# Optimization experiments

Hardware: AMD Instinct MI355X
Metric: run time of the kernel (lower is better)

## Reference

```python
import math
import jax, jax.numpy as jnp
import numpy as np

B, N, D, H = 8, 128, 256, 8
DK = D // H
SCALE = 0.02


def setup_inputs() -> dict:
    key = jax.random.key(0)
    ks = jax.random.split(key, 10)
    return {
        "query_node": jax.random.normal(ks[0], (B, N, D), jnp.float32),
        "value_node": jax.random.normal(ks[1], (B, N, D), jnp.float32),
        "key_edge": jax.random.normal(ks[2], (B, N, N, D), jnp.float32),
        "adj_matrix": jax.random.uniform(ks[3], (B, N, N), jnp.float32),  # pairwise distances >= 0
        "mask": jnp.ones((B, N), jnp.int32),
        "Wq": jax.random.normal(ks[4], (D, D), jnp.float32) * SCALE,
        "bq": jnp.zeros((D,), jnp.float32),
        "Wk": jax.random.normal(ks[5], (D, D), jnp.float32) * SCALE,
        "bk": jnp.zeros((D,), jnp.float32),
        "Wv": jax.random.normal(ks[6], (D, D), jnp.float32) * SCALE,
        "bv": jnp.zeros((D,), jnp.float32),
        "Wno": jax.random.normal(ks[7], (D, D), jnp.float32) * SCALE,
        "bno": jnp.zeros((D,), jnp.float32),
        "Weo": jax.random.normal(ks[8], (D, D), jnp.float32) * SCALE,
        "beo": jnp.zeros((D,), jnp.float32),
        "att_lambda": jnp.float32(0.1),
    }


def reference(query_node, value_node, key_edge, adj_matrix, mask,
              Wq, bq, Wk, bk, Wv, bv, Wno, bno, Weo, beo, att_lambda):
    # distance-kernelized adjacency: softmax(-lambda * dist) over neighbors
    adj = att_lambda * adj_matrix                                  # [B,N,N]
    adj = jnp.where(mask[:, None, :] == 0, jnp.inf, adj)
    adj = jax.nn.softmax(-adj, axis=-1)                            # [B,N,N]

    q = (query_node @ Wq.T + bq).reshape(B, N, H, DK).transpose(0, 2, 1, 3)      # [B,H,N,DK] bhmd
    k = (key_edge @ Wk.T + bk).reshape(B, N, N, H, DK).transpose(0, 3, 1, 2, 4)  # [B,H,N,N,DK] bhmnd
    v = (value_node @ Wv.T + bv).reshape(B, N, H, DK).transpose(0, 2, 1, 3)      # [B,H,N,DK] bhnd

    inv_sqrt = 1.0 / math.sqrt(DK)
    out_scores = jnp.einsum('bhmd,bhmnd->bhmn', q, k) * inv_sqrt
    in_scores = jnp.einsum('bhnd,bhmnd->bhnm', q, k) * inv_sqrt

    m4 = mask[:, None, None, :] == 0                               # [B,1,1,N]
    neg_inf = jnp.asarray(-jnp.inf, out_scores.dtype)
    out_scores = jnp.where(m4, neg_inf, out_scores)
    in_scores = jnp.where(m4, neg_inf, in_scores)

    out_attn = jax.nn.softmax(out_scores, axis=-1)
    in_attn = jax.nn.softmax(in_scores, axis=-1)

    # message = out_attn + in_attn - diag_embed(diag(out_attn))
    eye = jnp.eye(N, dtype=out_attn.dtype)
    message = out_attn + in_attn - out_attn * eye
    message = message * adj[:, None]                               # adjacency gating (dropout = identity at eval)

    node_hidden = jnp.einsum('bhmn,bhnd->bhmd', message, v)        # [B,H,N,DK]
    edge_hidden = message[..., None] * k                           # [B,H,N,N,DK] outer-product edge update

    node_hidden = node_hidden.transpose(0, 2, 1, 3).reshape(B, N, D)
    edge_hidden = edge_hidden.transpose(0, 2, 3, 1, 4).reshape(B, N, N, D)

    return (node_hidden @ Wno.T + bno, edge_hidden @ Weo.T + beo)
```

## Files before the change

kernel.cpp:

```cpp
#include <hip/hip_runtime.h>
#include <math.h>

#define Bc 8
#define Nc 128
#define Dc 256
#define Hc 8
#define DKc 32

typedef __attribute__((ext_vector_type(8))) short short8;
typedef __attribute__((ext_vector_type(4))) float floatx4;

__device__ __forceinline__ unsigned short f2bf(float f) {
  unsigned int u = __float_as_uint(f);
  u += 0x7FFFu + ((u >> 16) & 1u);
  return (unsigned short)(u >> 16);
}

__global__ __launch_bounds__(256) void cast_bf16_kernel(
    const float* __restrict__ src, unsigned short* __restrict__ dst, int n) {
  const int i = (blockIdx.x * 256 + threadIdx.x) * 4;
  if (i < n) {
    const float4 v = *(const float4*)&src[i];
    *(ushort4*)&dst[i] = make_ushort4(f2bf(v.x), f2bf(v.y), f2bf(v.z), f2bf(v.w));
  }
}

__global__ __launch_bounds__(256) void gemm_xwT_kernel(
    const float* __restrict__ X, const float* __restrict__ W,
    const float* __restrict__ bias, float* __restrict__ C, int M) {
  __shared__ float As[64][17];
  __shared__ float Ws[64][17];
  const int t = threadIdx.x;
  const int tx = t & 15;
  const int ty = t >> 4;
  const size_t row0 = (size_t)blockIdx.y * 64;
  const int col0 = blockIdx.x * 64;
  const int lr = t >> 2;
  const int lc = (t & 3) * 4;

  float acc[4][4] = {};

  for (int kk = 0; kk < 256; kk += 16) {
    float4 av = *(const float4*)&X[(row0 + lr) * 256 + kk + lc];
    float4 wv = *(const float4*)&W[(size_t)(col0 + lr) * 256 + kk + lc];
    As[lr][lc] = av.x; As[lr][lc + 1] = av.y; As[lr][lc + 2] = av.z; As[lr][lc + 3] = av.w;
    Ws[lr][lc] = wv.x; Ws[lr][lc + 1] = wv.y; Ws[lr][lc + 2] = wv.z; Ws[lr][lc + 3] = wv.w;
    __syncthreads();
#pragma unroll
    for (int e = 0; e < 16; ++e) {
      float a[4], w[4];
#pragma unroll
      for (int r = 0; r < 4; ++r) a[r] = As[ty * 4 + r][e];
#pragma unroll
      for (int c = 0; c < 4; ++c) w[c] = Ws[tx * 4 + c][e];
#pragma unroll
      for (int r = 0; r < 4; ++r)
#pragma unroll
        for (int c = 0; c < 4; ++c) acc[r][c] = fmaf(a[r], w[c], acc[r][c]);
    }
    __syncthreads();
  }

  const float4 bv = *(const float4*)&bias[col0 + tx * 4];
#pragma unroll
  for (int r = 0; r < 4; ++r) {
    float4 o;
    o.x = acc[r][0] + bv.x;
    o.y = acc[r][1] + bv.y;
    o.z = acc[r][2] + bv.z;
    o.w = acc[r][3] + bv.w;
    *(float4*)&C[(row0 + ty * 4 + r) * 256 + col0 + tx * 4] = o;
  }
}

__global__ __launch_bounds__(256) void kproj_mfma_kernel(
    const float* __restrict__ X, const unsigned short* __restrict__ Wbf,
    const float* __restrict__ bias, float* __restrict__ C) {
  __shared__ __align__(16) unsigned short As[128 * 40];
  __shared__ __align__(16) unsigned short Ws[128 * 40];
  const int t = threadIdx.x;
  const int l = t & 63;
  const int w = t >> 6;
  const int wm = w >> 1, wn = w & 1;
  const size_t row0 = (size_t)blockIdx.y * 128;
  const int col0 = blockIdx.x * 128;
  const int lr = l & 15;
  const int lk = l >> 4;

  floatx4 acc[4][4] = {};

  for (int kk = 0; kk < 256; kk += 32) {
    float4 av[4];
#pragma unroll
    for (int p = 0; p < 4; ++p) {
      const int f = p * 256 + t;
      const int row = f >> 3, kc = (f & 7) * 4;
      av[p] = *(const float4*)&X[(row0 + row) * 256 + kk + kc];
    }
    uint4 wv[2];
#pragma unroll
    for (int p = 0; p < 2; ++p) {
      const int f = p * 256 + t;
      const int row = f >> 2, kc = (f & 3) * 8;
      wv[p] = *(const uint4*)&Wbf[(size_t)(col0 + row) * 256 + kk + kc];
    }
    __syncthreads();
#pragma unroll
    for (int p = 0; p < 4; ++p) {
      const int f = p * 256 + t;
      const int row = f >> 3, kc = (f & 7) * 4;
      *(ushort4*)&As[row * 40 + kc] =
          make_ushort4(f2bf(av[p].x), f2bf(av[p].y), f2bf(av[p].z), f2bf(av[p].w));
    }
#pragma unroll
    for (int p = 0; p < 2; ++p) {
      const int f = p * 256 + t;
      const int row = f >> 2, kc = (f & 3) * 8;
      *(uint4*)&Ws[row * 40 + kc] = wv[p];
    }
    __syncthreads();
    short8 a[4], b[4];
#pragma unroll
    for (int i = 0; i < 4; ++i)
      a[i] = *(const short8*)&As[(wm * 64 + i * 16 + lr) * 40 + lk * 8];
#pragma unroll
    for (int j = 0; j < 4; ++j)
      b[j] = *(const short8*)&Ws[(wn * 64 + j * 16 + lr) * 40 + lk * 8];
#pragma unroll
    for (int i = 0; i < 4; ++i)
#pragma unroll
      for (int j = 0; j < 4; ++j)
        acc[i][j] = __builtin_amdgcn_mfma_f32_16x16x32_bf16(a[i], b[j], acc[i][j], 0, 0, 0);
  }

  float bj[4];
#pragma unroll
  for (int j = 0; j < 4; ++j) bj[j] = bias[col0 + wn * 64 + j * 16 + lr];
#pragma unroll
  for (int i = 0; i < 4; ++i)
#pragma unroll
    for (int r = 0; r < 4; ++r) {
      const size_t row = row0 + wm * 64 + i * 16 + lk * 4 + r;
#pragma unroll
      for (int j = 0; j < 4; ++j)
        C[row * 256 + col0 + wn * 64 + j * 16 + lr] = acc[i][j][r] + bj[j];
    }
}

__global__ __launch_bounds__(128) void adj_softmax_kernel(
    const float* __restrict__ adj, const int* __restrict__ mask,
    const float* __restrict__ lam_p, float* __restrict__ adjs) {
  __shared__ float red[128];
  const int bi = blockIdx.x;
  const int b = bi >> 7;
  const int j = threadIdx.x;
  const float lam = lam_p[0];
  float x = (mask[b * 128 + j] != 0) ? (-lam * adj[(size_t)bi * 128 + j]) : -INFINITY;
  red[j] = x; __syncthreads();
  for (int s = 64; s > 0; s >>= 1) { if (j < s) red[j] = fmaxf(red[j], red[j + s]); __syncthreads(); }
  const float mx = red[0]; __syncthreads();
  const float e = expf(x - mx);
  red[j] = e; __syncthreads();
  for (int s = 64; s > 0; s >>= 1) { if (j < s) red[j] += red[j + s]; __syncthreads(); }
  const float z = red[0];
  adjs[(size_t)bi * 128 + j] = e / z;
}

__global__ __launch_bounds__(256) void scores_kernel(
    const float* __restrict__ kbuf, const float* __restrict__ q,
    float* __restrict__ osc, float* __restrict__ isc) {
  const int bm = blockIdx.x;
  const int b = bm >> 7;
  const int m = bm & 127;
  const int lane = threadIdx.x & 63;
  const int wave = threadIdx.x >> 6;
  const float inv_sqrt = 0.17677669529663687f;

  const float4 qm = *(const float4*)&q[((size_t)b * 128 + m) * 256 + lane * 4];

  for (int n = wave; n < 128; n += 4) {
    const float4 kr = *(const float4*)&kbuf[((size_t)bm * 128 + n) * 256 + lane * 4];
    const float4 qn = *(const float4*)&q[((size_t)b * 128 + n) * 256 + lane * 4];
    float po = kr.x * qm.x + kr.y * qm.y + kr.z * qm.z + kr.w * qm.w;
    float pi = kr.x * qn.x + kr.y * qn.y + kr.z * qn.z + kr.w * qn.w;
#pragma unroll
    for (int off = 1; off < 8; off <<= 1) {
      po += __shfl_xor(po, off, 64);
      pi += __shfl_xor(pi, off, 64);
    }
    if ((lane & 7) == 0) {
      const int h = lane >> 3;
      osc[(((size_t)(b * 8 + h) * 128 + m) * 128) + n] = po * inv_sqrt;
      isc[(((size_t)(b * 8 + h) * 128 + n) * 128) + m] = pi * inv_sqrt;
    }
  }
}

__global__ __launch_bounds__(128) void message_kernel(
    const float* __restrict__ osc, const float* __restrict__ isc,
    const float* __restrict__ adjs, const int* __restrict__ mask,
    float* __restrict__ msg) {
  __shared__ float red[128];
  const int bhi = blockIdx.x;
  const int i = bhi & 127;
  const int b = bhi >> 10;
  const int j = threadIdx.x;
  const bool mj = mask[b * 128 + j] != 0;

  const float so = mj ? osc[(size_t)bhi * 128 + j] : -INFINITY;
  const float si = mj ? isc[(size_t)bhi * 128 + j] : -INFINITY;

  red[j] = so; __syncthreads();
  for (int s = 64; s > 0; s >>= 1) { if (j < s) red[j] = fmaxf(red[j], red[j + s]); __syncthreads(); }
  const float mo = red[0]; __syncthreads();
  const float eo = expf(so - mo);
  red[j] = eo; __syncthreads();
  for (int s = 64; s > 0; s >>= 1) { if (j < s) red[j] += red[j + s]; __syncthreads(); }
  const float zo = red[0]; __syncthreads();
  const float oa = eo / zo;

  red[j] = si; __syncthreads();
  for (int s = 64; s > 0; s >>= 1) { if (j < s) red[j] = fmaxf(red[j], red[j + s]); __syncthreads(); }
  const float mi = red[0]; __syncthreads();
  const float ei = expf(si - mi);
  red[j] = ei; __syncthreads();
  for (int s = 64; s > 0; s >>= 1) { if (j < s) red[j] += red[j + s]; __syncthreads(); }
  const float zi = red[0];
  const float ia = ei / zi;

  float val = oa + ia - ((i == j) ? oa : 0.0f);
  val *= adjs[((size_t)(b * 128 + i)) * 128 + j];
  msg[(size_t)bhi * 128 + j] = val;
}

__global__ __launch_bounds__(256) void node_hidden_kernel(
    const float* __restrict__ msg, const float* __restrict__ v,
    float* __restrict__ nh) {
  __shared__ float Ms[32][129];
  __shared__ float Vs[128][33];
  const int blk = blockIdx.x;
  const int mblk = blk & 3;
  const int bh = blk >> 2;
  const int h = bh & 7;
  const int b = bh >> 3;
  const int t = threadIdx.x;

  {
    const int n = t & 127, r0 = t >> 7;
#pragma unroll
    for (int p = 0; p < 16; ++p) {
      const int r = r0 + p * 2;
      Ms[r][n] = msg[((size_t)bh * 128 + mblk * 32 + r) * 128 + n];
    }
  }
  {
    const int dk = t & 31, n0 = t >> 5;
#pragma unroll
    for (int p = 0; p < 16; ++p) {
      const int n = n0 + p * 8;
      Vs[n][dk] = v[((size_t)b * 128 + n) * 256 + h * 32 + dk];
    }
  }
  __syncthreads();

  const int dk = t & 31;
  const int mg = t >> 5;
  float acc[4] = {0.f, 0.f, 0.f, 0.f};
  for (int n = 0; n < 128; ++n) {
    const float vv = Vs[n][dk];
#pragma unroll
    for (int r = 0; r < 4; ++r) acc[r] = fmaf(Ms[mg + 8 * r][n], vv, acc[r]);
  }
#pragma unroll
  for (int r = 0; r < 4; ++r) {
    const int m = mblk * 32 + mg + 8 * r;
    nh[((size_t)b * 128 + m) * 256 + h * 32 + dk] = acc[r];
  }
}

__global__ __launch_bounds__(256) void edge_mfma_kernel(
    float* __restrict__ kio, const float* __restrict__ msg,
    const unsigned short* __restrict__ Wbf, const float* __restrict__ beo) {
  __shared__ __align__(16) unsigned short As[64 * 40];
  __shared__ __align__(16) unsigned short Ws[256 * 40];
  __shared__ float Msgs[64][8];
  const int nblk = blockIdx.x;
  const int bm = blockIdx.y;
  const int b = bm >> 7;
  const int m = bm & 127;
  const int n0 = nblk * 64;
  const int t = threadIdx.x;
  const int l = t & 63;
  const int w = t >> 6;
  const int lr = l & 15;
  const int lk = l >> 4;

#pragma unroll
  for (int p = 0; p < 2; ++p) {
    const int idx = t + p * 256;
    const int r = idx >> 3, h = idx & 7;
    Msgs[r][h] = msg[(((size_t)(b * 8 + h) * 128 + m) * 128) + n0 + r];
  }
  __syncthreads();

  const size_t rowbase = ((size_t)bm * 128 + n0) * 256;
  floatx4 acc[4][4] = {};

  for (int kk = 0; kk < 256; kk += 32) {
    const int h = kk >> 5;
    float4 av[2];
    int arow[2];
#pragma unroll
    for (int p = 0; p < 2; ++p) {
      const int f = p * 256 + t;
      arow[p] = f >> 3;
      const int kc = (f & 7) * 4;
      av[p] = *(const float4*)&kio[rowbase + (size_t)arow[p] * 256 + kk + kc];
    }
    uint4 wv[4];
#pragma unroll
    for (int p = 0; p < 4; ++p) {
      const int f = p * 256 + t;
      const int row = f >> 2, kc = (f & 3) * 8;
      wv[p] = *(const uint4*)&Wbf[(size_t)row * 256 + kk + kc];
    }
    __syncthreads();
#pragma unroll
    for (int p = 0; p < 2; ++p) {
      const int f = p * 256 + t;
      const int kc = (f & 7) * 4;
      const float sc = Msgs[arow[p]][h];
      *(ushort4*)&As[arow[p] * 40 + kc] =
          make_ushort4(f2bf(av[p].x * sc), f2bf(av[p].y * sc),
                       f2bf(av[p].z * sc), f2bf(av[p].w * sc));
    }
#pragma unroll
    for (int p = 0; p < 4; ++p) {
      const int f = p * 256 + t;
      const int row = f >> 2, kc = (f & 3) * 8;
      *(uint4*)&Ws[row * 40 + kc] = wv[p];
    }
    __syncthreads();
    short8 a[4], bfr[4];
#pragma unroll
    for (int i = 0; i < 4; ++i)
      a[i] = *(const short8*)&As[(i * 16 + lr) * 40 + lk * 8];
#pragma unroll
    for (int j = 0; j < 4; ++j)
      bfr[j] = *(const short8*)&Ws[(w * 64 + j * 16 + lr) * 40 + lk * 8];
#pragma unroll
    for (int i = 0; i < 4; ++i)
#pragma unroll
      for (int j = 0; j < 4; ++j)
        acc[i][j] = __builtin_amdgcn_mfma_f32_16x16x32_bf16(a[i], bfr[j], acc[i][j], 0, 0, 0);
  }

  float bj[4];
#pragma unroll
  for (int j = 0; j < 4; ++j) bj[j] = beo[w * 64 + j * 16 + lr];
#pragma unroll
  for (int i = 0; i < 4; ++i)
#pragma unroll
    for (int r = 0; r < 4; ++r) {
      const size_t row = (size_t)(i * 16 + lk * 4 + r);
#pragma unroll
      for (int j = 0; j < 4; ++j)
        kio[rowbase + row * 256 + w * 64 + j * 16 + lr] = acc[i][j][r] + bj[j];
    }
}

extern "C" void kernel_launch(void* const* d_in, const int* in_sizes, int n_in,
                              void* d_out, int out_size, void* d_ws, size_t ws_size,
                              hipStream_t stream) {
  (void)in_sizes; (void)n_in; (void)out_size; (void)ws_size;
  const float* query_node = (const float*)d_in[0];
  const float* value_node = (const float*)d_in[1];
  const float* key_edge   = (const float*)d_in[2];
  const float* adj_matrix = (const float*)d_in[3];
  const int*   mask       = (const int*)d_in[4];
  const float* Wq  = (const float*)d_in[5];
  const float* bq  = (const float*)d_in[6];
  const float* Wk  = (const float*)d_in[7];
  const float* bk  = (const float*)d_in[8];
  const float* Wv  = (const float*)d_in[9];
  const float* bv  = (const float*)d_in[10];
  const float* Wno = (const float*)d_in[11];
  const float* bno = (const float*)d_in[12];
  const float* Weo = (const float*)d_in[13];
  const float* beo = (const float*)d_in[14];
  const float* lam = (const float*)d_in[15];

  float* out = (float*)d_out;
  float* node_out = out;
  float* kbuf = out + (size_t)Bc * Nc * Dc;

  float* ws = (float*)d_ws;
  float* q    = ws; ws += (size_t)Bc * Nc * Dc;
  float* v    = ws; ws += (size_t)Bc * Nc * Dc;
  float* adjs = ws; ws += (size_t)Bc * Nc * Nc;
  float* osc  = ws; ws += (size_t)Bc * Hc * Nc * Nc;
  float* isc  = ws; ws += (size_t)Bc * Hc * Nc * Nc;
  float* msg  = ws; ws += (size_t)Bc * Hc * Nc * Nc;
  float* nh   = ws; ws += (size_t)Bc * Nc * Dc;
  unsigned short* wkbf  = (unsigned short*)ws; ws += 32768;
  unsigned short* weobf = (unsigned short*)ws; ws += 32768;

  cast_bf16_kernel<<<dim3(64), 256, 0, stream>>>(Wk, wkbf, Dc * Dc);
  cast_bf16_kernel<<<dim3(64), 256, 0, stream>>>(Weo, weobf, Dc * Dc);
  gemm_xwT_kernel<<<dim3(4, 16), 256, 0, stream>>>(query_node, Wq, bq, q, Bc * Nc);
  gemm_xwT_kernel<<<dim3(4, 16), 256, 0, stream>>>(value_node, Wv, bv, v, Bc * Nc);
  kproj_mfma_kernel<<<dim3(2, 1024), 256, 0, stream>>>(key_edge, wkbf, bk, kbuf);
  adj_softmax_kernel<<<dim3(Bc * Nc), 128, 0, stream>>>(adj_matrix, mask, lam, adjs);
  scores_kernel<<<dim3(Bc * Nc), 256, 0, stream>>>(kbuf, q, osc, isc);
  message_kernel<<<dim3(Bc * Hc * Nc), 128, 0, stream>>>(osc, isc, adjs, mask, msg);
  node_hidden_kernel<<<dim3(Bc * Hc * 4), 256, 0, stream>>>(msg, v, nh);
  gemm_xwT_kernel<<<dim3(4, 16), 256, 0, stream>>>(nh, Wno, bno, node_out, Bc * Nc);
  edge_mfma_kernel<<<dim3(2, 1024), 256, 0, stream>>>(kbuf, msg, weobf, beo);
}
```

Measured before the change: 544.6 us.

## Fold Wk into query for scores and fuse K projection into edge GEMM

Scores are now computed directly against the raw key_edge by first projecting the queries through Wk per head (qw = q_h·Wk_h plus a bias term), so the materialized K tensor is no longer needed for the score pass. The K projection moves into the edge kernel. That kernel computes K for a tile in registers, scales it by the message, stages it in shared memory as bf16, and runs the Weo GEMM right away, so the large K buffer is never written to or re-read from global memory. The cost is a per-head qw workspace eight times larger than q, score reads of fp32 key_edge at full width, and extra LDS use for the K1 tile.

```diff
diff --git a/kernel.cpp b/kernel.cpp
--- a/kernel.cpp
+++ b/kernel.cpp
@@ -73,78 +73,28 @@
   }
 }
 
-__global__ __launch_bounds__(256) void kproj_mfma_kernel(
-    const float* __restrict__ X, const unsigned short* __restrict__ Wbf,
-    const float* __restrict__ bias, float* __restrict__ C) {
-  __shared__ __align__(16) unsigned short As[128 * 40];
-  __shared__ __align__(16) unsigned short Ws[128 * 40];
-  const int t = threadIdx.x;
-  const int l = t & 63;
-  const int w = t >> 6;
-  const int wm = w >> 1, wn = w & 1;
-  const size_t row0 = (size_t)blockIdx.y * 128;
-  const int col0 = blockIdx.x * 128;
-  const int lr = l & 15;
-  const int lk = l >> 4;
-
-  floatx4 acc[4][4] = {};
-
-  for (int kk = 0; kk < 256; kk += 32) {
-    float4 av[4];
-#pragma unroll
-    for (int p = 0; p < 4; ++p) {
-      const int f = p * 256 + t;
-      const int row = f >> 3, kc = (f & 7) * 4;
-      av[p] = *(const float4*)&X[(row0 + row) * 256 + kk + kc];
-    }
-    uint4 wv[2];
-#pragma unroll
-    for (int p = 0; p < 2; ++p) {
-      const int f = p * 256 + t;
-      const int row = f >> 2, kc = (f & 3) * 8;
-      wv[p] = *(const uint4*)&Wbf[(size_t)(col0 + row) * 256 + kk + kc];
-    }
-    __syncthreads();
-#pragma unroll
-    for (int p = 0; p < 4; ++p) {
-      const int f = p * 256 + t;
-      const int row = f >> 3, kc = (f & 7) * 4;
-      *(ushort4*)&As[row * 40 + kc] =
-          make_ushort4(f2bf(av[p].x), f2bf(av[p].y), f2bf(av[p].z), f2bf(av[p].w));
-    }
-#pragma unroll
-    for (int p = 0; p < 2; ++p) {
-      const int f = p * 256 + t;
-      const int row = f >> 2, kc = (f & 3) * 8;
-      *(uint4*)&Ws[row * 40 + kc] = wv[p];
-    }
-    __syncthreads();
-    short8 a[4], b[4];
-#pragma unroll
-    for (int i = 0; i < 4; ++i)
-      a[i] = *(const short8*)&As[(wm * 64 + i * 16 + lr) * 40 + lk * 8];
-#pragma unroll
-    for (int j = 0; j < 4; ++j)
-      b[j] = *(const short8*)&Ws[(wn * 64 + j * 16 + lr) * 40 + lk * 8];
-#pragma unroll
-    for (int i = 0; i < 4; ++i)
-#pragma unroll
-      for (int j = 0; j < 4; ++j)
-        acc[i][j] = __builtin_amdgcn_mfma_f32_16x16x32_bf16(a[i], b[j], acc[i][j], 0, 0, 0);
-  }
-
-  float bj[4];
-#pragma unroll
-  for (int j = 0; j < 4; ++j) bj[j] = bias[col0 + wn * 64 + j * 16 + lr];
-#pragma unroll
-  for (int i = 0; i < 4; ++i)
-#pragma unroll
-    for (int r = 0; r < 4; ++r) {
-      const size_t row = row0 + wm * 64 + i * 16 + lk * 4 + r;
-#pragma unroll
-      for (int j = 0; j < 4; ++j)
-        C[row * 256 + col0 + wn * 64 + j * 16 + lr] = acc[i][j][r] + bj[j];
-    }
+__global__ __launch_bounds__(256) void qw_kernel(
+    const float* __restrict__ q, const float* __restrict__ Wk,
+    const float* __restrict__ bk, float* __restrict__ qw,
+    float* __restrict__ qb) {
+  __shared__ float qs[256];
+  const int bm = blockIdx.x;
+  const int e = threadIdx.x;
+  qs[e] = q[(size_t)bm * 256 + e];
+  __syncthreads();
+  float acc[8] = {0.f, 0.f, 0.f, 0.f, 0.f, 0.f, 0.f, 0.f};
+  for (int d = 0; d < 32; ++d) {
+#pragma unroll
+    for (int h = 0; h < 8; ++h)
+      acc[h] = fmaf(qs[h * 32 + d], Wk[(size_t)(h * 32 + d) * 256 + e], acc[h]);
+  }
+#pragma unroll
+  for (int h = 0; h < 8; ++h) qw[((size_t)bm * 8 + h) * 256 + e] = acc[h];
+  if (e < 8) {
+    float s = 0.f;
+    for (int d = 0; d < 32; ++d) s = fmaf(qs[e * 32 + d], bk[e * 32 + d], s);
+    qb[(size_t)bm * 8 + e] = s;
+  }
 }
 
 __global__ __launch_bounds__(128) void adj_softmax_kernel(
@@ -166,32 +116,59 @@
   adjs[(size_t)bi * 128 + j] = e / z;
 }
 
-__global__ __launch_bounds__(256) void scores_kernel(
-    const float* __restrict__ kbuf, const float* __restrict__ q,
-    float* __restrict__ osc, float* __restrict__ isc) {
-  const int bm = blockIdx.x;
-  const int b = bm >> 7;
-  const int m = bm & 127;
+__global__ __launch_bounds__(256) void scores_qw_kernel(
+    const float* __restrict__ ke, const float* __restrict__ qw,
+    const float* __restrict__ qb, float* __restrict__ osc,
+    float* __restrict__ isc) {
+  const int bid = blockIdx.x;
+  const int swz = (bid & 7) * 64 + (bid >> 3);
+  const int b = swz >> 6;
+  const int m0 = (swz & 63) * 2;
   const int lane = threadIdx.x & 63;
   const int wave = threadIdx.x >> 6;
+  const int h = lane >> 3, s = lane & 7;
   const float inv_sqrt = 0.17677669529663687f;
 
-  const float4 qm = *(const float4*)&q[((size_t)b * 128 + m) * 256 + lane * 4];
+  float4 qma[8], qmb[8];
+  const size_t qbase0 = (((size_t)(b * 128 + m0)) * 8 + h) * 256 + s * 32;
+  const size_t qbase1 = qbase0 + 8 * 256;
+#pragma unroll
+  for (int f = 0; f < 8; ++f) {
+    qma[f] = *(const float4*)&qw[qbase0 + f * 4];
+    qmb[f] = *(const float4*)&qw[qbase1 + f * 4];
+  }
+  const float qbm0 = qb[(size_t)(b * 128 + m0) * 8 + h];
+  const float qbm1 = qb[(size_t)(b * 128 + m0 + 1) * 8 + h];
 
   for (int n = wave; n < 128; n += 4) {
-    const float4 kr = *(const float4*)&kbuf[((size_t)bm * 128 + n) * 256 + lane * 4];
-    const float4 qn = *(const float4*)&q[((size_t)b * 128 + n) * 256 + lane * 4];
-    float po = kr.x * qm.x + kr.y * qm.y + kr.z * qm.z + kr.w * qm.w;
-    float pi = kr.x * qn.x + kr.y * qn.y + kr.z * qn.z + kr.w * qn.w;
+    const size_t kr0 = (((size_t)(b * 128 + m0)) * 128 + n) * 256 + s * 32;
+    const size_t kr1 = kr0 + 128 * 256;
+    const size_t qnb = (((size_t)(b * 128 + n)) * 8 + h) * 256 + s * 32;
+    float po0 = 0.f, po1 = 0.f, pi0 = 0.f, pi1 = 0.f;
+#pragma unroll
+    for (int f = 0; f < 8; ++f) {
+      const float4 k0 = *(const float4*)&ke[kr0 + f * 4];
+      const float4 k1 = *(const float4*)&ke[kr1 + f * 4];
+      const float4 qn = *(const float4*)&qw[qnb + f * 4];
+      po0 = fmaf(k0.x, qma[f].x, fmaf(k0.y, qma[f].y, fmaf(k0.z, qma[f].z, fmaf(k0.w, qma[f].w, po0))));
+      po1 = fmaf(k1.x, qmb[f].x, fmaf(k1.y, qmb[f].y, fmaf(k1.z, qmb[f].z, fmaf(k1.w, qmb[f].w, po1))));
+      pi0 = fmaf(k0.x, qn.x, fmaf(k0.y, qn.y, fmaf(k0.z, qn.z, fmaf(k0.w, qn.w, pi0))));
+      pi1 = fmaf(k1.x, qn.x, fmaf(k1.y, qn.y, fmaf(k1.z, qn.z, fmaf(k1.w, qn.w, pi1))));
+    }
 #pragma unroll
     for (int off = 1; off < 8; off <<= 1) {
-      po += __shfl_xor(po, off, 64);
-      pi += __shfl_xor(pi, off, 64);
-    }
-    if ((lane & 7) == 0) {
-      const int h = lane >> 3;
-      osc[(((size_t)(b * 8 + h) * 128 + m) * 128) + n] = po * inv_sqrt;
-      isc[(((size_t)(b * 8 + h) * 128 + n) * 128) + m] = pi * inv_sqrt;
+      po0 += __shfl_xor(po0, off, 64);
+      po1 += __shfl_xor(po1, off, 64);
+      pi0 += __shfl_xor(pi0, off, 64);
+      pi1 += __shfl_xor(pi1, off, 64);
+    }
+    if (s == 0) {
+      const float qbn = qb[(size_t)(b * 128 + n) * 8 + h];
+      const size_t hb = (size_t)(b * 8 + h) * 128;
+      osc[(hb + m0) * 128 + n]     = (po0 + qbm0) * inv_sqrt;
+      osc[(hb + m0 + 1) * 128 + n] = (po1 + qbm1) * inv_sqrt;
+      isc[(hb + n) * 128 + m0]     = (pi0 + qbn) * inv_sqrt;
+      isc[(hb + n) * 128 + m0 + 1] = (pi1 + qbn) * inv_sqrt;
     }
   }
 }
@@ -278,11 +255,14 @@
   }
 }
 
-__global__ __launch_bounds__(256) void edge_mfma_kernel(
-    float* __restrict__ kio, const float* __restrict__ msg,
-    const unsigned short* __restrict__ Wbf, const float* __restrict__ beo) {
+__global__ __launch_bounds__(256) void edge_fused_kernel(
+    const float* __restrict__ ke, const float* __restrict__ msg,
+    const unsigned short* __restrict__ wk, const unsigned short* __restrict__ weo,
+    const float* __restrict__ bk, const float* __restrict__ beo,
+    float* __restrict__ out) {
   __shared__ __align__(16) unsigned short As[64 * 40];
   __shared__ __align__(16) unsigned short Ws[256 * 40];
+  __shared__ __align__(16) unsigned short K1[64 * 264];
   __shared__ float Msgs[64][8];
   const int nblk = blockIdx.x;
   const int bm = blockIdx.y;
@@ -294,6 +274,7 @@
   const int w = t >> 6;
   const int lr = l & 15;
   const int lk = l >> 4;
+  const size_t rowbase = ((size_t)bm * 128 + n0) * 256;
 
 #pragma unroll
   for (int p = 0; p < 2; ++p) {
@@ -301,39 +282,29 @@
     const int r = idx >> 3, h = idx & 7;
     Msgs[r][h] = msg[(((size_t)(b * 8 + h) * 128 + m) * 128) + n0 + r];
   }
-  __syncthreads();
-
-  const size_t rowbase = ((size_t)bm * 128 + n0) * 256;
+
   floatx4 acc[4][4] = {};
 
   for (int kk = 0; kk < 256; kk += 32) {
-    const int h = kk >> 5;
-    float4 av[2];
-    int arow[2];
+    float4 av[2]; int arow[2], akc[2];
 #pragma unroll
     for (int p = 0; p < 2; ++p) {
       const int f = p * 256 + t;
-      arow[p] = f >> 3;
-      const int kc = (f & 7) * 4;
-      av[p] = *(const float4*)&kio[rowbase + (size_t)arow[p] * 256 + kk + kc];
+      arow[p] = f >> 3; akc[p] = (f & 7) * 4;
+      av[p] = *(const float4*)&ke[rowbase + (size_t)arow[p] * 256 + kk + akc[p]];
     }
     uint4 wv[4];
 #pragma unroll
     for (int p = 0; p < 4; ++p) {
       const int f = p * 256 + t;
       const int row = f >> 2, kc = (f & 3) * 8;
-      wv[p] = *(const uint4*)&Wbf[(size_t)row * 256 + kk + kc];
-    }
-    __syncthreads();
-#pragma unroll
-    for (int p = 0; p < 2; ++p) {
-      const int f = p * 256 + t;
-      const int kc = (f & 7) * 4;
-      const float sc = Msgs[arow[p]][h];
-      *(ushort4*)&As[arow[p] * 40 + kc] =
-          make_ushort4(f2bf(av[p].x * sc), f2bf(av[p].y * sc),
-                       f2bf(av[p].z * sc), f2bf(av[p].w * sc));
-    }
+      wv[p] = *(const uint4*)&wk[(size_t)row * 256 + kk + kc];
+    }
+    __syncthreads();
+#pragma unroll
+    for (int p = 0; p < 2; ++p)
+      *(ushort4*)&As[arow[p] * 40 + akc[p]] =
+          make_ushort4(f2bf(av[p].x), f2bf(av[p].y), f2bf(av[p].z), f2bf(av[p].w));
 #pragma unroll
     for (int p = 0; p < 4; ++p) {
       const int f = p * 256 + t;
@@ -341,32 +312,83 @@
       *(uint4*)&Ws[row * 40 + kc] = wv[p];
     }
     __syncthreads();
-    short8 a[4], bfr[4];
+    short8 a[4], bw[4];
 #pragma unroll
     for (int i = 0; i < 4; ++i)
       a[i] = *(const short8*)&As[(i * 16 + lr) * 40 + lk * 8];
 #pragma unroll
     for (int j = 0; j < 4; ++j)
-      bfr[j] = *(const short8*)&Ws[(w * 64 + j * 16 + lr) * 40 + lk * 8];
+      bw[j] = *(const short8*)&Ws[(w * 64 + j * 16 + lr) * 40 + lk * 8];
 #pragma unroll
     for (int i = 0; i < 4; ++i)
 #pragma unroll
       for (int j = 0; j < 4; ++j)
-        acc[i][j] = __builtin_amdgcn_mfma_f32_16x16x32_bf16(a[i], bfr[j], acc[i][j], 0, 0, 0);
-  }
-
-  float bj[4];
-#pragma unroll
-  for (int j = 0; j < 4; ++j) bj[j] = beo[w * 64 + j * 16 + lr];
-#pragma unroll
-  for (int i = 0; i < 4; ++i)
-#pragma unroll
-    for (int r = 0; r < 4; ++r) {
-      const size_t row = (size_t)(i * 16 + lk * 4 + r);
+        acc[i][j] = __builtin_amdgcn_mfma_f32_16x16x32_bf16(bw[j], a[i], acc[i][j], 0, 0, 0);
+  }
+
+#pragma unroll
+  for (int j = 0; j < 4; ++j) {
+    const int col = w * 64 + j * 16 + lk * 4;
+    const float4 kb = *(const float4*)&bk[col];
+    const int h = col >> 5;
+#pragma unroll
+    for (int i = 0; i < 4; ++i) {
+      const int row = i * 16 + lr;
+      const float sc = Msgs[row][h];
+      *(ushort4*)&K1[row * 264 + col] = make_ushort4(
+          f2bf((acc[i][j][0] + kb.x) * sc), f2bf((acc[i][j][1] + kb.y) * sc),
+          f2bf((acc[i][j][2] + kb.z) * sc), f2bf((acc[i][j][3] + kb.w) * sc));
+      acc[i][j] = (floatx4){0.f, 0.f, 0.f, 0.f};
+    }
+  }
+  __syncthreads();
+
+  for (int kk = 0; kk < 256; kk += 32) {
+    uint4 wv[4];
+#pragma unroll
+    for (int p = 0; p < 4; ++p) {
+      const int f = p * 256 + t;
+      const int row = f >> 2, kc = (f & 3) * 8;
+      wv[p] = *(const uint4*)&weo[(size_t)row * 256 + kk + kc];
+    }
+    __syncthreads();
+#pragma unroll
+    for (int p = 0; p < 4; ++p) {
+      const int f = p * 256 + t;
+      const int row = f >> 2, kc = (f & 3) * 8;
+      *(uint4*)&Ws[row * 40 + kc] = wv[p];
+    }
+    __syncthreads();
+    short8 ak[4], bw[4];
+#pragma unroll
+    for (int i = 0; i < 4; ++i)
+      ak[i] = *(const short8*)&K1[(i * 16 + lr) * 264 + kk + lk * 8];
+#pragma unroll
+    for (int j = 0; j < 4; ++j)
+      bw[j] = *(const short8*)&Ws[(w * 64 + j * 16 + lr) * 40 + lk * 8];
+#pragma unroll
+    for (int i = 0; i < 4; ++i)
 #pragma unroll
       for (int j = 0; j < 4; ++j)
-        kio[rowbase + row * 256 + w * 64 + j * 16 + lr] = acc[i][j][r] + bj[j];
-    }
+        acc[i][j] = __builtin_amdgcn_mfma_f32_16x16x32_bf16(bw[j], ak[i], acc[i][j], 0, 0, 0);
+  }
+
+  float4 bj[4];
+#pragma unroll
+  for (int j = 0; j < 4; ++j) bj[j] = *(const float4*)&beo[w * 64 + j * 16 + lk * 4];
+#pragma unroll
+  for (int i = 0; i < 4; ++i) {
+    const size_t rb = rowbase + (size_t)(i * 16 + lr) * 256;
+#pragma unroll
+    for (int j = 0; j < 4; ++j) {
+      float4 o;
+      o.x = acc[i][j][0] + bj[j].x;
+      o.y = acc[i][j][1] + bj[j].y;
+      o.z = acc[i][j][2] + bj[j].z;
+      o.w = acc[i][j][3] + bj[j].w;
+      *(float4*)&out[rb + w * 64 + j * 16 + lk * 4] = o;
+    }
+  }
 }
 
 extern "C" void kernel_launch(void* const* d_in, const int* in_sizes, int n_in,
@@ -392,7 +414,7 @@
 
   float* out = (float*)d_out;
   float* node_out = out;
-  float* kbuf = out + (size_t)Bc * Nc * Dc;
+  float* edge_out = out + (size_t)Bc * Nc * Dc;
 
   float* ws = (float*)d_ws;
   float* q    = ws; ws += (size_t)Bc * Nc * Dc;
@@ -402,6 +424,8 @@
   float* isc  = ws; ws += (size_t)Bc * Hc * Nc * Nc;
   float* msg  = ws; ws += (size_t)Bc * Hc * Nc * Nc;
   float* nh   = ws; ws += (size_t)Bc * Nc * Dc;
+  float* qw   = ws; ws += (size_t)Bc * Nc * Hc * Dc;
+  float* qb   = ws; ws += (size_t)Bc * Nc * Hc;
   unsigned short* wkbf  = (unsigned short*)ws; ws += 32768;
   unsigned short* weobf = (unsigned short*)ws; ws += 32768;
 
@@ -409,11 +433,12 @@
   cast_bf16_kernel<<<dim3(64), 256, 0, stream>>>(Weo, weobf, Dc * Dc);
   gemm_xwT_kernel<<<dim3(4, 16), 256, 0, stream>>>(query_node, Wq, bq, q, Bc * Nc);
   gemm_xwT_kernel<<<dim3(4, 16), 256, 0, stream>>>(value_node, Wv, bv, v, Bc * Nc);
-  kproj_mfma_kernel<<<dim3(2, 1024), 256, 0, stream>>>(key_edge, wkbf, bk, kbuf);
+  qw_kernel<<<dim3(Bc * Nc), 256, 0, stream>>>(q, Wk, bk, qw, qb);
   adj_softmax_kernel<<<dim3(Bc * Nc), 128, 0, stream>>>(adj_matrix, mask, lam, adjs);
-  scores_kernel<<<dim3(Bc * Nc), 256, 0, stream>>>(kbuf, q, osc, isc);
+  scores_qw_kernel<<<dim3(512), 256, 0, stream>>>(key_edge, qw, qb, osc, isc);
   message_kernel<<<dim3(Bc * Hc * Nc), 128, 0, stream>>>(osc, isc, adjs, mask, msg);
   node_hidden_kernel<<<dim3(Bc * Hc * 4), 256, 0, stream>>>(msg, v, nh);
   gemm_xwT_kernel<<<dim3(4, 16), 256, 0, stream>>>(nh, Wno, bno, node_out, Bc * Nc);
-  edge_mfma_kernel<<<dim3(2, 1024), 256, 0, stream>>>(kbuf, msg, weobf, beo);
-}
+  edge_fused_kernel<<<dim3(2, 1024), 256, 0, stream>>>(
+      key_edge, msg, wkbf, weobf, bk, beo, edge_out);
+}
```

Measured after the change: 686.7 us. 1.26x slower.
